# Kernel tuning notes

Measured on AMD Instinct MI355X. Metric: run time of the kernel, lower is better.

## Reference

```python
import jax, jax.numpy as jnp
import numpy as np

B, T, C = 4, 1024, 1024
H = 16
DH = C // H  # 64


def setup_inputs() -> dict:
    key = jax.random.key(0)
    ks = jax.random.split(key, 10)
    s = 0.02
    return {
        "x": jax.random.normal(ks[0], (B, T, C), dtype=jnp.float32),
        "Wq": jax.random.normal(ks[1], (C, C), dtype=jnp.float32) * s,
        "bq": jnp.zeros((C,), dtype=jnp.float32),
        "Wk": jax.random.normal(ks[2], (C, C), dtype=jnp.float32) * s,
        "bk": jnp.zeros((C,), dtype=jnp.float32),
        "Wv": jax.random.normal(ks[3], (C, C), dtype=jnp.float32) * s,
        "bv": jnp.zeros((C,), dtype=jnp.float32),
        "Wp": jax.random.normal(ks[4], (C, C), dtype=jnp.float32) * s,
        "bp": jnp.zeros((C,), dtype=jnp.float32),
    }


def reference(x, Wq, bq, Wk, bk, Wv, bv, Wp, bp):
    b, t, c = x.shape
    # QKV projections, split into heads: [b, H, t, DH]
    def heads(y):
        return y.reshape(b, t, H, DH).transpose(0, 2, 1, 3)
    q = heads(x @ Wq + bq)
    k = heads(x @ Wk + bk)
    v = heads(x @ Wv + bv)
    # Causal attention. Original masks with -inf BEFORE scaling; -inf*scale is
    # still -inf, so mask-then-scale == scale-then-mask.
    scores = jnp.einsum("bhqd,bhkd->bhqk", q, k) * (DH ** -0.5)
    causal = jnp.tril(jnp.ones((t, t), dtype=bool))
    scores = jnp.where(causal, scores, -jnp.inf)
    attn = jax.nn.softmax(scores, axis=-1)  # dropout p=0.0 -> identity
    ctx = jnp.einsum("bhqk,bhkd->bhqd", attn, v)
    ctx = ctx.transpose(0, 2, 1, 3).reshape(b, t, c)
    return ctx @ Wp + bp
```

## Files before the change

kernel.cpp:

```cpp
#include <hip/hip_runtime.h>


typedef unsigned short ushort_t;
typedef __attribute__((ext_vector_type(8))) __bf16 bf16x8;
typedef __attribute__((ext_vector_type(8))) unsigned short us8;
typedef __attribute__((ext_vector_type(4))) unsigned short us4;
typedef __attribute__((ext_vector_type(4))) float f32x4;

#define AS1 __attribute__((address_space(1)))
#define AS3 __attribute__((address_space(3)))

__device__ __forceinline__ ushort_t f2bf(float f) {
  unsigned int u = __float_as_uint(f);
  u += 0x7fffu + ((u >> 16) & 1u);
  return (ushort_t)(u >> 16);
}


__global__ void cvt_x_kernel(const float* __restrict__ x, ushort_t* __restrict__ xb) {
  const int i = blockIdx.x * 256 + threadIdx.x;
  const float4 v = reinterpret_cast<const float4*>(x)[i];
  us4 o;
  o.x = f2bf(v.x); o.y = f2bf(v.y); o.z = f2bf(v.z); o.w = f2bf(v.w);
  reinterpret_cast<us4*>(xb)[i] = o;
}

__global__ void cvt_w4_kernel(const float* __restrict__ Wq, const float* __restrict__ Wk,
                              const float* __restrict__ Wv, const float* __restrict__ Wp,
                              ushort_t* __restrict__ WQKVT, ushort_t* __restrict__ WPT) {
  __shared__ float t[32][33];
  const int z = blockIdx.z;
  const float* W = (z == 0) ? Wq : (z == 1) ? Wk : (z == 2) ? Wv : Wp;
  ushort_t* Wt = (z == 3) ? WPT : (WQKVT + ((size_t)z << 20));
  const float wscale = (z == 0) ? 0.125f : 1.0f;
  const int n0 = blockIdx.x * 32, k0 = blockIdx.y * 32;
  const int tx = threadIdx.x, ty = threadIdx.y;
#pragma unroll
  for (int i = ty; i < 32; i += 8)
    t[i][tx] = W[(size_t)(k0 + i) * 1024 + n0 + tx];
  __syncthreads();
#pragma unroll
  for (int i = ty; i < 32; i += 8)
    Wt[(size_t)(n0 + i) * 1024 + k0 + tx] = f2bf(t[tx][i] * wscale);
}


__global__ __launch_bounds__(512, 2) void gemm_qkv256_kernel(
    const ushort_t* __restrict__ A, const ushort_t* __restrict__ Bt,
    const float* __restrict__ bq, const float* __restrict__ bk,
    const float* __restrict__ bv, ushort_t* __restrict__ QKVB,
    ushort_t* __restrict__ VT) {
  __shared__ ushort_t smem[2][2][256 * 32];
  const int tid = threadIdx.x;
  const int wave = tid >> 6, lane = tid & 63;
  const int lgrp = lane >> 4, lmod = lane & 15;
  const int wr = wave >> 2, wc = wave & 3;
  const int swz = (blockIdx.x & 7) * 24 + (blockIdx.x >> 3);
  const int row0 = (swz / 12) * 256, col0 = (swz % 12) * 256;

  const ushort_t* Ag = A + (size_t)row0 * 1024;
  const ushort_t* Bg = Bt + (size_t)col0 * 1024;

  auto stage8k = [&](ushort_t* reg, const ushort_t* g0, int i) {
    const int row = i * 128 + wave * 16 + (lane >> 2);
    const int cb = (lane & 3) << 4;
    __builtin_amdgcn_global_load_lds(
        (AS1 void*)(g0 + (size_t)row * 1024 + (cb >> 1)),
        (AS3 void*)((char*)reg + i * 8192 + wave * 1024), 16, 0, 0);
  };

  f32x4 acc[8][4] = {};
  constexpr int nt = 32;

  stage8k(&smem[0][0][0], Ag, 0);
  stage8k(&smem[0][0][0], Ag, 1);
  stage8k(&smem[0][1][0], Bg, 0);
  stage8k(&smem[0][1][0], Bg, 1);

  for (int t = 0; t < nt; ++t) {
    const int cur = t & 1, nxt = cur ^ 1;
    const char* curA = (const char*)&smem[cur][0][0];
    const char* curB = (const char*)&smem[cur][1][0];
    if (t + 1 < nt) {
      stage8k(&smem[nxt][0][0], Ag + (t + 1) * 32, 0);
      stage8k(&smem[nxt][0][0], Ag + (t + 1) * 32, 1);
      asm volatile("s_waitcnt vmcnt(2)" ::: "memory");
    } else {
      asm volatile("s_waitcnt vmcnt(0)" ::: "memory");
    }
    __builtin_amdgcn_sched_barrier(0);
    __builtin_amdgcn_s_barrier();

    bf16x8 bfr[4], af[4];
#pragma unroll
    for (int ni = 0; ni < 4; ++ni)
      bfr[ni] = *reinterpret_cast<const bf16x8*>(
          curB + (wc * 64 + ni * 16 + lmod) * 64 + lgrp * 16);
#pragma unroll
    for (int mi = 0; mi < 4; ++mi)
      af[mi] = *reinterpret_cast<const bf16x8*>(
          curA + (wr * 128 + mi * 16 + lmod) * 64 + lgrp * 16);
    if (t + 1 < nt) {
      stage8k(&smem[nxt][1][0], Bg + (t + 1) * 32, 0);
      stage8k(&smem[nxt][1][0], Bg + (t + 1) * 32, 1);
    }
    __builtin_amdgcn_s_setprio(1);
#pragma unroll
    for (int mi = 0; mi < 4; ++mi)
#pragma unroll
      for (int ni = 0; ni < 4; ++ni)
        acc[mi][ni] = __builtin_amdgcn_mfma_f32_16x16x32_bf16(af[mi], bfr[ni], acc[mi][ni], 0, 0, 0);
    __builtin_amdgcn_s_setprio(0);
    __builtin_amdgcn_s_barrier();

#pragma unroll
    for (int mi = 0; mi < 4; ++mi)
      af[mi] = *reinterpret_cast<const bf16x8*>(
          curA + (wr * 128 + (4 + mi) * 16 + lmod) * 64 + lgrp * 16);
    __builtin_amdgcn_s_setprio(1);
#pragma unroll
    for (int mi = 0; mi < 4; ++mi)
#pragma unroll
      for (int ni = 0; ni < 4; ++ni)
        acc[4 + mi][ni] = __builtin_amdgcn_mfma_f32_16x16x32_bf16(af[mi], bfr[ni], acc[4 + mi][ni], 0, 0, 0);
    __builtin_amdgcn_s_setprio(0);
    __builtin_amdgcn_s_barrier();
  }

  if (col0 < 2048) {
    const float* bsel = (col0 < 1024) ? bq : bk;
    const float bsc = (col0 < 1024) ? 0.125f : 1.0f;
    float bvv[4];
#pragma unroll
    for (int ni = 0; ni < 4; ++ni)
      bvv[ni] = bsel[(col0 & 1023) + wc * 64 + ni * 16 + lmod] * bsc;
#pragma unroll
    for (int mi = 0; mi < 8; ++mi) {
#pragma unroll
      for (int ni = 0; ni < 4; ++ni) {
        const int col = col0 + wc * 64 + ni * 16 + lmod;
#pragma unroll
        for (int r = 0; r < 4; ++r) {
          const int row = row0 + wr * 128 + mi * 16 + lgrp * 4 + r;
          QKVB[(size_t)row * 3072 + col] = f2bf(acc[mi][ni][r] + bvv[ni]);
        }
      }
    }
  } else {
    float bvv[4];
#pragma unroll
    for (int ni = 0; ni < 4; ++ni)
      bvv[ni] = bv[(col0 - 2048) + wc * 64 + ni * 16 + lmod];
#pragma unroll
    for (int mi = 0; mi < 8; ++mi) {
#pragma unroll
      for (int ni = 0; ni < 4; ++ni) {
        const int hd = (col0 - 2048) + wc * 64 + ni * 16 + lmod;
        const int R = row0 + wr * 128 + mi * 16 + lgrp * 4;
        const int bb = R >> 10, tl = R & 1023;
        us4 o;
#pragma unroll
        for (int r = 0; r < 4; ++r) o[r] = f2bf(acc[mi][ni][r] + bvv[ni]);
        *reinterpret_cast<us4*>(VT + ((size_t)(bb * 16 + (hd >> 6)) * 64 + (hd & 63)) * 1024 + tl) = o;
      }
    }
  }
}


__global__ __launch_bounds__(256, 2) void gemm_proj_kernel(
    const ushort_t* __restrict__ A, const ushort_t* __restrict__ Bt,
    const float* __restrict__ bias, float* __restrict__ Cout) {
  constexpr int BM = 64, WR = 32, MFR = 2, NIT = 3;
  __shared__ ushort_t As[BM * 32];
  __shared__ ushort_t Bs[128 * 32];
  const int tid = threadIdx.x;
  const int wave = tid >> 6, lane = tid & 63;
  const int lgrp = lane >> 4, lmod = lane & 15;
  const int wr = wave >> 1, wc = wave & 1;
  const int cpx = gridDim.x >> 3;
  const int swz = (blockIdx.x & 7) * cpx + (blockIdx.x >> 3);
  const int row0 = (swz / 8) * BM, col0 = (swz % 8) * 128;

  f32x4 acc[MFR][4] = {};

  for (int k0 = 0; k0 < 1024; k0 += 32) {
#pragma unroll
    for (int it = 0; it < NIT; ++it) {
      const int c0 = it * 256 + wave * 64;
      const int c = c0 + lane;
      if (c0 < BM * 4) {
        const int r = c >> 2, kk = (c & 3) << 3;
        __builtin_amdgcn_global_load_lds(
            (AS1 void*)(A + (size_t)(row0 + r) * 1024 + k0 + kk),
            (AS3 void*)(As + (c0 << 3)), 16, 0, 0);
      } else {
        const int cb = c - BM * 4;
        const int r = cb >> 2, kk = (cb & 3) << 3;
        __builtin_amdgcn_global_load_lds(
            (AS1 void*)(Bt + (size_t)(col0 + r) * 1024 + k0 + kk),
            (AS3 void*)(Bs + ((c0 - BM * 4) << 3)), 16, 0, 0);
      }
    }
    __syncthreads();

    bf16x8 af[MFR], bfr[4];
#pragma unroll
    for (int i = 0; i < MFR; ++i)
      af[i] = *reinterpret_cast<const bf16x8*>(&As[(wr * WR + i * 16 + lmod) * 32 + lgrp * 8]);
#pragma unroll
    for (int i = 0; i < 4; ++i)
      bfr[i] = *reinterpret_cast<const bf16x8*>(&Bs[(wc * 64 + i * 16 + lmod) * 32 + lgrp * 8]);
    __builtin_amdgcn_s_setprio(1);
#pragma unroll
    for (int mi = 0; mi < MFR; ++mi)
#pragma unroll
      for (int ni = 0; ni < 4; ++ni)
        acc[mi][ni] = __builtin_amdgcn_mfma_f32_16x16x32_bf16(af[mi], bfr[ni], acc[mi][ni], 0, 0, 0);
    __builtin_amdgcn_s_setprio(0);
    __syncthreads();
  }

  float bvv[4];
#pragma unroll
  for (int ni = 0; ni < 4; ++ni) bvv[ni] = bias[col0 + wc * 64 + ni * 16 + lmod];
#pragma unroll
  for (int mi = 0; mi < MFR; ++mi)
#pragma unroll
    for (int ni = 0; ni < 4; ++ni) {
      const int col = col0 + wc * 64 + ni * 16 + lmod;
#pragma unroll
      for (int r = 0; r < 4; ++r) {
        const int row = row0 + wr * WR + mi * 16 + lgrp * 4 + r;
        Cout[(size_t)row * 1024 + col] = acc[mi][ni][r] + bvv[ni];
      }
    }
}


__global__ __launch_bounds__(256, 2) void attn_kernel(
    const ushort_t* __restrict__ QKV, const ushort_t* __restrict__ VT,
    ushort_t* __restrict__ Og) {
  const int bid = blockIdx.x;
  const int swz = (bid & 7) * 64 + (bid >> 3);
  const int p = swz & 7, bh = swz >> 3;
  const int b = bh >> 4, h = bh & 15;
  const int jmax = 15 - p;
  const int tid = threadIdx.x;
  const int wave = tid >> 6, lane = tid & 63;
  const int lgrp = lane >> 4, lmod = lane & 15;

  __shared__ ushort_t Ks[64 * 72];
  __shared__ ushort_t Vs[64 * 72];
  __shared__ ushort_t Ps[4][16 * 72];

  const size_t xrow0 = (size_t)b * 1024;
  const int qlo = p * 64 + wave * 16;
  const int qhi = jmax * 64 + wave * 16;

  bf16x8 qfl[2], qfh[2];
#pragma unroll
  for (int ks = 0; ks < 2; ++ks) {
    qfl[ks] = *reinterpret_cast<const bf16x8*>(
        QKV + (xrow0 + qlo + lmod) * 3072 + h * 64 + ks * 32 + lgrp * 8);
    qfh[ks] = *reinterpret_cast<const bf16x8*>(
        QKV + (xrow0 + qhi + lmod) * 3072 + h * 64 + ks * 32 + lgrp * 8);
  }

  f32x4 ol[4] = {}, oh[4] = {};
  float ll[4] = {0.f, 0.f, 0.f, 0.f}, lh[4] = {0.f, 0.f, 0.f, 0.f};

  const int sr = tid >> 3;
  const int scc = (tid & 7) << 3;
  us8 kreg0, kreg1, vreg0, vreg1;

  auto load_tile = [&](int j) {
    const ushort_t* kp = QKV + (xrow0 + j * 64 + sr) * 3072 + 1024 + h * 64 + scc;
    kreg0 = *reinterpret_cast<const us8*>(kp);
    kreg1 = *reinterpret_cast<const us8*>(kp + 32 * 3072);
    const ushort_t* vp = VT + ((size_t)bh * 64 + sr) * 1024 + j * 64 + scc;
    vreg0 = *reinterpret_cast<const us8*>(vp);
    vreg1 = *reinterpret_cast<const us8*>(vp + 32 * 1024);
  };
  auto write_tile = [&]() {
    *reinterpret_cast<us8*>(&Ks[sr * 72 + scc]) = kreg0;
    *reinterpret_cast<us8*>(&Ks[(32 + sr) * 72 + scc]) = kreg1;
    *reinterpret_cast<us8*>(&Vs[sr * 72 + scc]) = vreg0;
    *reinterpret_cast<us8*>(&Vs[(32 + sr) * 72 + scc]) = vreg1;
  };

  auto step = [&](const bf16x8* qf, f32x4* oacc, float* lsum, bool diag) {
    f32x4 s[4];
    __builtin_amdgcn_s_setprio(1);
#pragma unroll
    for (int cg = 0; cg < 4; ++cg) {
      f32x4 a = {};
#pragma unroll
      for (int ks = 0; ks < 2; ++ks) {
        bf16x8 kf = *reinterpret_cast<const bf16x8*>(
            &Ks[(cg * 16 + lmod) * 72 + ks * 32 + lgrp * 8]);
        a = __builtin_amdgcn_mfma_f32_16x16x32_bf16(qf[ks], kf, a, 0, 0, 0);
      }
      s[cg] = a;
    }
    __builtin_amdgcn_s_setprio(0);
    if (diag) {
      const int qloc = wave * 16 + lgrp * 4;
#pragma unroll
      for (int cg = 0; cg < 4; ++cg) {
        const int kcol = cg * 16 + lmod;
#pragma unroll
        for (int r = 0; r < 4; ++r)
          if (kcol > qloc + r) s[cg][r] = -1e30f;
      }
    }
#pragma unroll
    for (int cg = 0; cg < 4; ++cg)
#pragma unroll
      for (int r = 0; r < 4; ++r) s[cg][r] = __expf(s[cg][r]);
#pragma unroll
    for (int r = 0; r < 4; ++r)
      lsum[r] += (s[0][r] + s[1][r]) + (s[2][r] + s[3][r]);
#pragma unroll
    for (int cg = 0; cg < 4; ++cg)
#pragma unroll
      for (int r = 0; r < 4; ++r)
        Ps[wave][(lgrp * 4 + r) * 72 + cg * 16 + lmod] = f2bf(s[cg][r]);
    __builtin_amdgcn_s_setprio(1);
#pragma unroll
    for (int ks = 0; ks < 2; ++ks) {
      bf16x8 pf = *reinterpret_cast<const bf16x8*>(
          &Ps[wave][lmod * 72 + ks * 32 + lgrp * 8]);
#pragma unroll
      for (int dhg = 0; dhg < 4; ++dhg) {
        bf16x8 vf = *reinterpret_cast<const bf16x8*>(
            &Vs[(dhg * 16 + lmod) * 72 + ks * 32 + lgrp * 8]);
        oacc[dhg] = __builtin_amdgcn_mfma_f32_16x16x32_bf16(pf, vf, oacc[dhg], 0, 0, 0);
      }
    }
    __builtin_amdgcn_s_setprio(0);
  };

  load_tile(0);
  for (int j = 0; j <= jmax; ++j) {
    __syncthreads();
    write_tile();
    __syncthreads();
    if (j < jmax) load_tile(j + 1);
    if (j <= p) step(qfl, ol, ll, j == p);
    step(qfh, oh, lh, j == jmax);
  }

#pragma unroll
  for (int m = 1; m <= 8; m <<= 1)
#pragma unroll
    for (int r = 0; r < 4; ++r) {
      ll[r] += __shfl_xor(ll[r], m);
      lh[r] += __shfl_xor(lh[r], m);
    }

#pragma unroll
  for (int dhg = 0; dhg < 4; ++dhg) {
    const int col = h * 64 + dhg * 16 + lmod;
#pragma unroll
    for (int r = 0; r < 4; ++r) {
      Og[(xrow0 + qlo + lgrp * 4 + r) * 1024 + col] = f2bf(ol[dhg][r] / ll[r]);
      Og[(xrow0 + qhi + lgrp * 4 + r) * 1024 + col] = f2bf(oh[dhg][r] / lh[r]);
    }
  }
}


extern "C" void kernel_launch(void* const* d_in, const int* in_sizes, int n_in,
                              void* d_out, int out_size, void* d_ws, size_t ws_size,
                              hipStream_t stream) {
  const float* x  = (const float*)d_in[0];
  const float* Wq = (const float*)d_in[1];
  const float* bq = (const float*)d_in[2];
  const float* Wk = (const float*)d_in[3];
  const float* bk = (const float*)d_in[4];
  const float* Wv = (const float*)d_in[5];
  const float* bv = (const float*)d_in[6];
  const float* Wp = (const float*)d_in[7];
  const float* bp = (const float*)d_in[8];
  float* out = (float*)d_out;

  char* ws = (char*)d_ws;
  ushort_t* XB    = (ushort_t*)(ws);
  ushort_t* WQKVT = (ushort_t*)(ws + ( 8ull << 20));
  ushort_t* WPT   = (ushort_t*)(ws + (14ull << 20));
  ushort_t* QKVB  = (ushort_t*)(ws + (16ull << 20));
  ushort_t* VT    = (ushort_t*)(ws + (40ull << 20));

  cvt_x_kernel<<<4096, 256, 0, stream>>>(x, XB);
  cvt_w4_kernel<<<dim3(32, 32, 4), dim3(32, 8), 0, stream>>>(Wq, Wk, Wv, Wp, WQKVT, WPT);
  gemm_qkv256_kernel<<<192, 512, 0, stream>>>(XB, WQKVT, bq, bk, bv, QKVB, VT);
  attn_kernel<<<512, 256, 0, stream>>>(QKVB, VT, XB);
  gemm_proj_kernel<<<512, 256, 0, stream>>>(XB, WPT, bp, out);
}
```

Before: 98.40 us.

## Double QKV GEMM K-tile to 64 with XOR-swizzled LDS and split staging

The QKV GEMM now stages 64-wide K slices instead of 32, halving the loop iterations and barrier-bounded phases per K. LDS is written with an XOR swizzle on 16-byte slots, and fragment reads apply the matching swizzle to avoid bank conflicts. The next tile's loads are split into two halves issued at different points in the iteration. The LDS footprint doubles to 128KB and the min-blocks-per-CU hint is dropped, which likely limits occupancy to one 512-thread block per CU.

```diff
diff --git a/kernel.cpp b/kernel.cpp
--- a/kernel.cpp
+++ b/kernel.cpp
@@ -45,12 +45,12 @@
 }
 
 
-__global__ __launch_bounds__(512, 2) void gemm_qkv256_kernel(
+__global__ __launch_bounds__(512) void gemm_qkv256_kernel(
     const ushort_t* __restrict__ A, const ushort_t* __restrict__ Bt,
     const float* __restrict__ bq, const float* __restrict__ bk,
     const float* __restrict__ bv, ushort_t* __restrict__ QKVB,
     ushort_t* __restrict__ VT) {
-  __shared__ ushort_t smem[2][2][256 * 32];
+  __shared__ ushort_t smem[2][2][256 * 64];
   const int tid = threadIdx.x;
   const int wave = tid >> 6, lane = tid & 63;
   const int lgrp = lane >> 4, lmod = lane & 15;
@@ -61,68 +61,103 @@
   const ushort_t* Ag = A + (size_t)row0 * 1024;
   const ushort_t* Bg = Bt + (size_t)col0 * 1024;
 
-  auto stage8k = [&](ushort_t* reg, const ushort_t* g0, int i) {
-    const int row = i * 128 + wave * 16 + (lane >> 2);
-    const int cb = (lane & 3) << 4;
-    __builtin_amdgcn_global_load_lds(
-        (AS1 void*)(g0 + (size_t)row * 1024 + (cb >> 1)),
-        (AS3 void*)((char*)reg + i * 8192 + wave * 1024), 16, 0, 0);
+  const int srow = lane >> 3;
+  const int sslot = (lane & 7) ^ srow;
+  const int xm = lmod & 7;
+
+  auto stage_half = [&](int buf, int t, int h) {
+#pragma unroll
+    for (int op = 0; op < 2; ++op) {
+      const ushort_t* G = (op ? Bg : Ag) + t * 64;
+#pragma unroll
+      for (int i = 0; i < 2; ++i) {
+        const int c0 = h * 1024 + i * 512 + wave * 64;
+        __builtin_amdgcn_global_load_lds(
+            (AS1 void*)(G + (size_t)((c0 >> 3) + srow) * 1024 + sslot * 8),
+            (AS3 void*)((char*)&smem[buf][op][0] + c0 * 16), 16, 0, 0);
+      }
+    }
   };
 
   f32x4 acc[8][4] = {};
-  constexpr int nt = 32;
-
-  stage8k(&smem[0][0][0], Ag, 0);
-  stage8k(&smem[0][0][0], Ag, 1);
-  stage8k(&smem[0][1][0], Bg, 0);
-  stage8k(&smem[0][1][0], Bg, 1);
+  constexpr int nt = 16;
+
+  stage_half(0, 0, 0);
+  stage_half(0, 0, 1);
 
   for (int t = 0; t < nt; ++t) {
     const int cur = t & 1, nxt = cur ^ 1;
-    const char* curA = (const char*)&smem[cur][0][0];
-    const char* curB = (const char*)&smem[cur][1][0];
+    const char* cA = (const char*)&smem[cur][0][0];
+    const char* cB = (const char*)&smem[cur][1][0];
+
     if (t + 1 < nt) {
-      stage8k(&smem[nxt][0][0], Ag + (t + 1) * 32, 0);
-      stage8k(&smem[nxt][0][0], Ag + (t + 1) * 32, 1);
-      asm volatile("s_waitcnt vmcnt(2)" ::: "memory");
+      stage_half(nxt, t + 1, 0);
+      asm volatile("s_waitcnt vmcnt(4)" ::: "memory");
     } else {
       asm volatile("s_waitcnt vmcnt(0)" ::: "memory");
     }
     __builtin_amdgcn_sched_barrier(0);
     __builtin_amdgcn_s_barrier();
 
-    bf16x8 bfr[4], af[4];
+    bf16x8 b0[4], b1[4], af[4];
 #pragma unroll
     for (int ni = 0; ni < 4; ++ni)
-      bfr[ni] = *reinterpret_cast<const bf16x8*>(
-          curB + (wc * 64 + ni * 16 + lmod) * 64 + lgrp * 16);
+      b0[ni] = *reinterpret_cast<const bf16x8*>(
+          cB + (wc * 64 + ni * 16 + lmod) * 128 + ((lgrp ^ xm) << 4));
 #pragma unroll
     for (int mi = 0; mi < 4; ++mi)
       af[mi] = *reinterpret_cast<const bf16x8*>(
-          curA + (wr * 128 + mi * 16 + lmod) * 64 + lgrp * 16);
-    if (t + 1 < nt) {
-      stage8k(&smem[nxt][1][0], Bg + (t + 1) * 32, 0);
-      stage8k(&smem[nxt][1][0], Bg + (t + 1) * 32, 1);
-    }
+          cA + (wr * 128 + mi * 16 + lmod) * 128 + ((lgrp ^ xm) << 4));
     __builtin_amdgcn_s_setprio(1);
 #pragma unroll
     for (int mi = 0; mi < 4; ++mi)
 #pragma unroll
       for (int ni = 0; ni < 4; ++ni)
-        acc[mi][ni] = __builtin_amdgcn_mfma_f32_16x16x32_bf16(af[mi], bfr[ni], acc[mi][ni], 0, 0, 0);
+        acc[mi][ni] = __builtin_amdgcn_mfma_f32_16x16x32_bf16(af[mi], b0[ni], acc[mi][ni], 0, 0, 0);
     __builtin_amdgcn_s_setprio(0);
     __builtin_amdgcn_s_barrier();
 
+    if (t + 1 < nt) stage_half(nxt, t + 1, 1);
 #pragma unroll
     for (int mi = 0; mi < 4; ++mi)
       af[mi] = *reinterpret_cast<const bf16x8*>(
-          curA + (wr * 128 + (4 + mi) * 16 + lmod) * 64 + lgrp * 16);
+          cA + (wr * 128 + (4 + mi) * 16 + lmod) * 128 + ((lgrp ^ xm) << 4));
     __builtin_amdgcn_s_setprio(1);
 #pragma unroll
     for (int mi = 0; mi < 4; ++mi)
 #pragma unroll
       for (int ni = 0; ni < 4; ++ni)
-        acc[4 + mi][ni] = __builtin_amdgcn_mfma_f32_16x16x32_bf16(af[mi], bfr[ni], acc[4 + mi][ni], 0, 0, 0);
+        acc[4 + mi][ni] = __builtin_amdgcn_mfma_f32_16x16x32_bf16(af[mi], b0[ni], acc[4 + mi][ni], 0, 0, 0);
+    __builtin_amdgcn_s_setprio(0);
+    __builtin_amdgcn_s_barrier();
+
+#pragma unroll
+    for (int ni = 0; ni < 4; ++ni)
+      b1[ni] = *reinterpret_cast<const bf16x8*>(
+          cB + (wc * 64 + ni * 16 + lmod) * 128 + (((4 | lgrp) ^ xm) << 4));
+#pragma unroll
+    for (int mi = 0; mi < 4; ++mi)
+      af[mi] = *reinterpret_cast<const bf16x8*>(
+          cA + (wr * 128 + mi * 16 + lmod) * 128 + (((4 | lgrp) ^ xm) << 4));
+    __builtin_amdgcn_s_setprio(1);
+#pragma unroll
+    for (int mi = 0; mi < 4; ++mi)
+#pragma unroll
+      for (int ni = 0; ni < 4; ++ni)
+        acc[mi][ni] = __builtin_amdgcn_mfma_f32_16x16x32_bf16(af[mi], b1[ni], acc[mi][ni], 0, 0, 0);
+    __builtin_amdgcn_s_setprio(0);
+    __builtin_amdgcn_s_barrier();
+
+#pragma unroll
+    for (int mi = 0; mi < 4; ++mi)
+      af[mi] = *reinterpret_cast<const bf16x8*>(
+          cA + (wr * 128 + (4 + mi) * 16 + lmod) * 128 + (((4 | lgrp) ^ xm) << 4));
+    __builtin_amdgcn_s_setprio(1);
+#pragma unroll
+    for (int mi = 0; mi < 4; ++mi)
+#pragma unroll
+      for (int ni = 0; ni < 4; ++ni)
+        acc[4 + mi][ni] = __builtin_amdgcn_mfma_f32_16x16x32_bf16(af[mi], b1[ni], acc[4 + mi][ni], 0, 0, 0);
     __builtin_amdgcn_s_setprio(0);
     __builtin_amdgcn_s_barrier();
   }
```

Result: faster. 96.09 us (-2.3%).

## Replace 256-tile QKV GEMM with swizzled 128-tile single-buffer kernel; use hardware bf16 convert

Applied to the files above, without the earlier changes.

The QKV projection GEMM moves from 256x256 tiles (192 blocks, 512 threads, double-buffered K=32) to 128x128 tiles (768 blocks, 256 threads) with K=64 steps and an XOR-swizzled LDS layout that avoids bank conflicts. The aim is to fill all 256 CUs, since 192 blocks leave many idle. The cost is losing the load/compute overlap of double buffering, because each step now waits for its loads to finish, and more global traffic from the smaller tiles. The attention kernel also switches its bf16 conversions from manual rounding to the compiler/hardware conversion.

```diff
diff --git a/kernel.cpp b/kernel.cpp
--- a/kernel.cpp
+++ b/kernel.cpp
@@ -14,6 +14,12 @@
   unsigned int u = __float_as_uint(f);
   u += 0x7fffu + ((u >> 16) & 1u);
   return (ushort_t)(u >> 16);
+}
+
+__device__ __forceinline__ ushort_t f2bf_hw(float f) {
+  union { __bf16 b; ushort_t u; } cv;
+  cv.b = (__bf16)f;
+  return cv.u;
 }
 
 
@@ -45,89 +51,75 @@
 }
 
 
-__global__ __launch_bounds__(512, 2) void gemm_qkv256_kernel(
+__global__ __launch_bounds__(256, 3) void gemm_qkv128_kernel(
     const ushort_t* __restrict__ A, const ushort_t* __restrict__ Bt,
     const float* __restrict__ bq, const float* __restrict__ bk,
     const float* __restrict__ bv, ushort_t* __restrict__ QKVB,
     ushort_t* __restrict__ VT) {
-  __shared__ ushort_t smem[2][2][256 * 32];
+  __shared__ ushort_t As[128 * 64];
+  __shared__ ushort_t Bs[128 * 64];
   const int tid = threadIdx.x;
   const int wave = tid >> 6, lane = tid & 63;
   const int lgrp = lane >> 4, lmod = lane & 15;
-  const int wr = wave >> 2, wc = wave & 3;
-  const int swz = (blockIdx.x & 7) * 24 + (blockIdx.x >> 3);
-  const int row0 = (swz / 12) * 256, col0 = (swz % 12) * 256;
-
-  const ushort_t* Ag = A + (size_t)row0 * 1024;
-  const ushort_t* Bg = Bt + (size_t)col0 * 1024;
-
-  auto stage8k = [&](ushort_t* reg, const ushort_t* g0, int i) {
-    const int row = i * 128 + wave * 16 + (lane >> 2);
-    const int cb = (lane & 3) << 4;
-    __builtin_amdgcn_global_load_lds(
-        (AS1 void*)(g0 + (size_t)row * 1024 + (cb >> 1)),
-        (AS3 void*)((char*)reg + i * 8192 + wave * 1024), 16, 0, 0);
+  const int wr = wave >> 1, wc = wave & 1;
+  const int swz = (blockIdx.x & 7) * 96 + (blockIdx.x >> 3);
+  const int rowt = swz / 24, colt = swz % 24;
+  const int row0 = rowt * 128, col0 = colt * 128;
+  const bool isV = (colt >= 16);
+
+  const int sslot = (tid & 7) ^ ((tid >> 3) & 7);
+  const int srow = tid >> 3;
+
+  auto stage = [&](int t) {
+    const ushort_t* Asrc = A + (size_t)row0 * 1024 + t * 64 + sslot * 8;
+    const ushort_t* Bsrc = Bt + (size_t)col0 * 1024 + t * 64 + sslot * 8;
+#pragma unroll
+    for (int i = 0; i < 4; ++i) {
+      __builtin_amdgcn_global_load_lds(
+          (AS1 void*)(Asrc + (size_t)(i * 32 + srow) * 1024),
+          (AS3 void*)(As + (i * 256 + wave * 64) * 8), 16, 0, 0);
+      __builtin_amdgcn_global_load_lds(
+          (AS1 void*)(Bsrc + (size_t)(i * 32 + srow) * 1024),
+          (AS3 void*)(Bs + (i * 256 + wave * 64) * 8), 16, 0, 0);
+    }
   };
 
-  f32x4 acc[8][4] = {};
-  constexpr int nt = 32;
-
-  stage8k(&smem[0][0][0], Ag, 0);
-  stage8k(&smem[0][0][0], Ag, 1);
-  stage8k(&smem[0][1][0], Bg, 0);
-  stage8k(&smem[0][1][0], Bg, 1);
-
-  for (int t = 0; t < nt; ++t) {
-    const int cur = t & 1, nxt = cur ^ 1;
-    const char* curA = (const char*)&smem[cur][0][0];
-    const char* curB = (const char*)&smem[cur][1][0];
-    if (t + 1 < nt) {
-      stage8k(&smem[nxt][0][0], Ag + (t + 1) * 32, 0);
-      stage8k(&smem[nxt][0][0], Ag + (t + 1) * 32, 1);
-      asm volatile("s_waitcnt vmcnt(2)" ::: "memory");
-    } else {
-      asm volatile("s_waitcnt vmcnt(0)" ::: "memory");
-    }
-    __builtin_amdgcn_sched_barrier(0);
+  f32x4 acc[4][4] = {};
+  const int xm = lmod & 7;
+
+  for (int t = 0; t < 16; ++t) {
+    stage(t);
+    asm volatile("s_waitcnt vmcnt(0)" ::: "memory");
     __builtin_amdgcn_s_barrier();
 
-    bf16x8 bfr[4], af[4];
+    bf16x8 af[4][2], bfr[4][2];
+#pragma unroll
+    for (int mi = 0; mi < 4; ++mi)
+#pragma unroll
+      for (int ks = 0; ks < 2; ++ks)
+        af[mi][ks] = *reinterpret_cast<const bf16x8*>(
+            &As[(wr * 64 + mi * 16 + lmod) * 64 + (((ks << 2) | lgrp) ^ xm) * 8]);
 #pragma unroll
     for (int ni = 0; ni < 4; ++ni)
-      bfr[ni] = *reinterpret_cast<const bf16x8*>(
-          curB + (wc * 64 + ni * 16 + lmod) * 64 + lgrp * 16);
+#pragma unroll
+      for (int ks = 0; ks < 2; ++ks)
+        bfr[ni][ks] = *reinterpret_cast<const bf16x8*>(
+            &Bs[(wc * 64 + ni * 16 + lmod) * 64 + (((ks << 2) | lgrp) ^ xm) * 8]);
+
+    __builtin_amdgcn_s_setprio(1);
 #pragma unroll
     for (int mi = 0; mi < 4; ++mi)
-      af[mi] = *reinterpret_cast<const bf16x8*>(
-          curA + (wr * 128 + mi * 16 + lmod) * 64 + lgrp * 16);
-    if (t + 1 < nt) {
-      stage8k(&smem[nxt][1][0], Bg + (t + 1) * 32, 0);
-      stage8k(&smem[nxt][1][0], Bg + (t + 1) * 32, 1);
-    }
-    __builtin_amdgcn_s_setprio(1);
-#pragma unroll
-    for (int mi = 0; mi < 4; ++mi)
 #pragma unroll
       for (int ni = 0; ni < 4; ++ni)
-        acc[mi][ni] = __builtin_amdgcn_mfma_f32_16x16x32_bf16(af[mi], bfr[ni], acc[mi][ni], 0, 0, 0);
+#pragma unroll
+        for (int ks = 0; ks < 2; ++ks)
+          acc[mi][ni] = __builtin_amdgcn_mfma_f32_16x16x32_bf16(
+              af[mi][ks], bfr[ni][ks], acc[mi][ni], 0, 0, 0);
     __builtin_amdgcn_s_setprio(0);
     __builtin_amdgcn_s_barrier();
-
-#pragma unroll
-    for (int mi = 0; mi < 4; ++mi)
-      af[mi] = *reinterpret_cast<const bf16x8*>(
-          curA + (wr * 128 + (4 + mi) * 16 + lmod) * 64 + lgrp * 16);
-    __builtin_amdgcn_s_setprio(1);
-#pragma unroll
-    for (int mi = 0; mi < 4; ++mi)
-#pragma unroll
-      for (int ni = 0; ni < 4; ++ni)
-        acc[4 + mi][ni] = __builtin_amdgcn_mfma_f32_16x16x32_bf16(af[mi], bfr[ni], acc[4 + mi][ni], 0, 0, 0);
-    __builtin_amdgcn_s_setprio(0);
-    __builtin_amdgcn_s_barrier();
-  }
-
-  if (col0 < 2048) {
+  }
+
+  if (!isV) {
     const float* bsel = (col0 < 1024) ? bq : bk;
     const float bsc = (col0 < 1024) ? 0.125f : 1.0f;
     float bvv[4];
@@ -135,13 +127,13 @@
     for (int ni = 0; ni < 4; ++ni)
       bvv[ni] = bsel[(col0 & 1023) + wc * 64 + ni * 16 + lmod] * bsc;
 #pragma unroll
-    for (int mi = 0; mi < 8; ++mi) {
+    for (int mi = 0; mi < 4; ++mi) {
 #pragma unroll
       for (int ni = 0; ni < 4; ++ni) {
         const int col = col0 + wc * 64 + ni * 16 + lmod;
 #pragma unroll
         for (int r = 0; r < 4; ++r) {
-          const int row = row0 + wr * 128 + mi * 16 + lgrp * 4 + r;
+          const int row = row0 + wr * 64 + mi * 16 + lgrp * 4 + r;
           QKVB[(size_t)row * 3072 + col] = f2bf(acc[mi][ni][r] + bvv[ni]);
         }
       }
@@ -152,11 +144,11 @@
     for (int ni = 0; ni < 4; ++ni)
       bvv[ni] = bv[(col0 - 2048) + wc * 64 + ni * 16 + lmod];
 #pragma unroll
-    for (int mi = 0; mi < 8; ++mi) {
+    for (int mi = 0; mi < 4; ++mi) {
 #pragma unroll
       for (int ni = 0; ni < 4; ++ni) {
         const int hd = (col0 - 2048) + wc * 64 + ni * 16 + lmod;
-        const int R = row0 + wr * 128 + mi * 16 + lgrp * 4;
+        const int R = row0 + wr * 64 + mi * 16 + lgrp * 4;
         const int bb = R >> 10, tl = R & 1023;
         us4 o;
 #pragma unroll
@@ -325,7 +317,7 @@
     for (int cg = 0; cg < 4; ++cg)
 #pragma unroll
       for (int r = 0; r < 4; ++r)
-        Ps[wave][(lgrp * 4 + r) * 72 + cg * 16 + lmod] = f2bf(s[cg][r]);
+        Ps[wave][(lgrp * 4 + r) * 72 + cg * 16 + lmod] = f2bf_hw(s[cg][r]);
     __builtin_amdgcn_s_setprio(1);
 #pragma unroll
     for (int ks = 0; ks < 2; ++ks) {
@@ -364,8 +356,8 @@
     const int col = h * 64 + dhg * 16 + lmod;
 #pragma unroll
     for (int r = 0; r < 4; ++r) {
-      Og[(xrow0 + qlo + lgrp * 4 + r) * 1024 + col] = f2bf(ol[dhg][r] / ll[r]);
-      Og[(xrow0 + qhi + lgrp * 4 + r) * 1024 + col] = f2bf(oh[dhg][r] / lh[r]);
+      Og[(xrow0 + qlo + lgrp * 4 + r) * 1024 + col] = f2bf_hw(ol[dhg][r] / ll[r]);
+      Og[(xrow0 + qhi + lgrp * 4 + r) * 1024 + col] = f2bf_hw(oh[dhg][r] / lh[r]);
     }
   }
 }
@@ -394,7 +386,7 @@
 
   cvt_x_kernel<<<4096, 256, 0, stream>>>(x, XB);
   cvt_w4_kernel<<<dim3(32, 32, 4), dim3(32, 8), 0, stream>>>(Wq, Wk, Wv, Wp, WQKVT, WPT);
-  gemm_qkv256_kernel<<<192, 512, 0, stream>>>(XB, WQKVT, bq, bk, bv, QKVB, VT);
+  gemm_qkv128_kernel<<<768, 256, 0, stream>>>(XB, WQKVT, bq, bk, bv, QKVB, VT);
   attn_kernel<<<512, 256, 0, stream>>>(QKVB, VT, XB);
   gemm_proj_kernel<<<512, 256, 0, stream>>>(XB, WPT, bp, out);
 }
```

New measurement: 89.08 us. -9.5%, faster.
